# Kernel tuning notes

Hardware: AMD Instinct MI355X
Metric: run time of the kernel (lower is better)

## Reference

```python
import jax, jax.numpy as jnp
import numpy as np

N_BITS = 6
N_ENTRIES = 1 << N_BITS  # 64 LUT entries per node
B, IN, OUT = 1024, 1024, 2048


def setup_inputs() -> dict:
    key = jax.random.key(0)
    k1, k2, k3 = jax.random.split(key, 3)
    x = jax.random.uniform(k1, (B, IN), dtype=jnp.float32)          # soft bits in [0,1]
    lut_table = jax.random.normal(k2, (OUT, N_ENTRIES), dtype=jnp.float32)  # per-node LUT weights
    mapping = jax.random.randint(k3, (OUT, N_BITS), 0, IN, dtype=jnp.int32)  # wires per node
    return {"x": x, "lut_table": lut_table, "mapping": mapping}


def _lut_forward(x, lut_table, mapping):
    # get_mapping: gather n input wires per output node -> [B, OUT, n]
    mapped = x[:, mapping]
    # bits[k, j] = j-th bit of entry k  -> [2^n, n]
    bits = ((jnp.arange(N_ENTRIES)[:, None] >> jnp.arange(N_BITS)[None, :]) & 1
            ).astype(x.dtype)
    # Soft-AND probability of each LUT entry, built multiplicatively over the
    # n (=6) fan-in bits to avoid a [B,OUT,2^n,n] intermediate.
    probs = jnp.ones((x.shape[0], mapping.shape[0], N_ENTRIES), dtype=x.dtype)
    for j in range(N_BITS):
        xj = mapped[:, :, j][:, :, None]              # [B, OUT, 1]
        bj = bits[:, j][None, None, :]                # [1, 1, 2^n]
        probs = probs * (bj * xj + (1.0 - bj) * (1.0 - xj))
    # Expected LUT output per node: contract entry axis with learned table.
    return jnp.einsum('bok,ok->bo', probs, lut_table)


def reference(x, lut_table, mapping):
    return _lut_forward(x, lut_table, mapping)
```

## Files before the change

kernel.cpp:

```cpp
#include <hip/hip_runtime.h>

#define B_DIM   1024
#define IN_DIM  1024
#define OUT_DIM 2048
#define NBITS   6
#define NENT    64

#define OB   256
#define BB   16
#define LROW 65

__global__ __launch_bounds__(256, 2) void lut_fused(
    const float* __restrict__ x,
    const float* __restrict__ lut,
    const int*   __restrict__ mapping,
    float*       __restrict__ out)
{
    __shared__ __align__(16) float smem[OB * LROW];
    const int tid = threadIdx.x;
    const int o0  = blockIdx.x * OB;
    const int b0  = blockIdx.y * BB;
    const int o   = o0 + tid;

    const float4* lsrc = (const float4*)(lut + (size_t)o0 * NENT);
#pragma unroll
    for (int i = 0; i < (OB * NENT / 4) / 256; i++) {
        const int f   = i * 256 + tid;
        const float4 val = lsrc[f];
        const int ow  = f >> 4;
        const int kw  = (f & 15) * 4;
        float* d = &smem[ow * LROW + kw];
        d[0] = val.x; d[1] = val.y; d[2] = val.z; d[3] = val.w;
    }

    int mp[NBITS];
#pragma unroll
    for (int j = 0; j < NBITS; j++) mp[j] = mapping[(size_t)o * NBITS + j];

    __syncthreads();

    float v[NENT];
#pragma unroll
    for (int k = 0; k < NENT; k++) v[k] = smem[tid * LROW + k];

#pragma unroll
    for (int j = 0; j < NBITS; j++) {
#pragma unroll
        for (int k = 0; k < NENT; k++) {
            if ((k >> j) & 1) v[k] -= v[k ^ (1 << j)];
        }
    }

    __syncthreads();

    const float4* xsrc = (const float4*)(x + (size_t)b0 * IN_DIM);
    float4* xdst = (float4*)smem;
#pragma unroll
    for (int i = 0; i < (BB * IN_DIM / 4) / 256; i++) {
        const int f = i * 256 + tid;
        xdst[f] = xsrc[f];
    }
    __syncthreads();

#pragma unroll 4
    for (int bi = 0; bi < BB; bi++) {
        const float* xr = &smem[bi * IN_DIM];
        float xv[NBITS];
#pragma unroll
        for (int j = 0; j < NBITS; j++) xv[j] = xr[mp[j]];

        float w[NENT / 2];
        {
            const float xj = xv[0];
#pragma unroll
            for (int m = 0; m < NENT / 2; m++)
                w[m] = fmaf(xj, v[2 * m + 1], v[2 * m]);
        }
#pragma unroll
        for (int j = 1; j < NBITS; j++) {
            const float xj = xv[j];
#pragma unroll
            for (int m = 0; m < (NENT >> (j + 1)); m++)
                w[m] = fmaf(xj, w[2 * m + 1], w[2 * m]);
        }
        out[(size_t)(b0 + bi) * OUT_DIM + o] = w[0];
    }
}

extern "C" void kernel_launch(void* const* d_in, const int* in_sizes, int n_in,
                              void* d_out, int out_size, void* d_ws, size_t ws_size,
                              hipStream_t stream) {
    const float* x       = (const float*)d_in[0];
    const float* lut     = (const float*)d_in[1];
    const int*   mapping = (const int*)d_in[2];
    float*       out     = (float*)d_out;
    (void)d_ws; (void)ws_size;

    const dim3 grid(OUT_DIM / OB, B_DIM / BB);
    lut_fused<<<grid, 256, 0, stream>>>(x, lut, mapping, out);
}
```

Measured before the change: 69.45 us.

## Load LUT rows directly into registers and overlap x staging with transform

Each thread now reads its own 64-entry LUT row straight from global memory as float4 into registers, so the padded shared-memory staging of the table and one barrier are gone. The x tile copy into shared memory is issued first so it overlaps with the LUT load and the per-thread Möbius transform, leaving one sync. Shared memory per block shrinks, and the batch loop unroll drops from 4 to 2. The per-thread row reads are strided across lanes (256 B apart), which may coalesce worse than the old cooperative copy.

Measured after the change: 70.93 us. 2.1% more time.

```diff
diff --git a/kernel.cpp b/kernel.cpp
--- a/kernel.cpp
+++ b/kernel.cpp
@@ -8,7 +8,6 @@
 
 #define OB   256
 #define BB   16
-#define LROW 65
 
 __global__ __launch_bounds__(256, 2) void lut_fused(
     const float* __restrict__ x,
@@ -16,32 +15,34 @@
     const int*   __restrict__ mapping,
     float*       __restrict__ out)
 {
-    __shared__ __align__(16) float smem[OB * LROW];
+    __shared__ __align__(16) float sx[BB * IN_DIM];
     const int tid = threadIdx.x;
     const int o0  = blockIdx.x * OB;
     const int b0  = blockIdx.y * BB;
     const int o   = o0 + tid;
 
-    const float4* lsrc = (const float4*)(lut + (size_t)o0 * NENT);
+    const float4* xsrc = (const float4*)(x + (size_t)b0 * IN_DIM);
+    float4* xdst = (float4*)sx;
 #pragma unroll
-    for (int i = 0; i < (OB * NENT / 4) / 256; i++) {
-        const int f   = i * 256 + tid;
-        const float4 val = lsrc[f];
-        const int ow  = f >> 4;
-        const int kw  = (f & 15) * 4;
-        float* d = &smem[ow * LROW + kw];
-        d[0] = val.x; d[1] = val.y; d[2] = val.z; d[3] = val.w;
+    for (int i = 0; i < (BB * IN_DIM / 4) / OB; i++) {
+        const int f = i * OB + tid;
+        xdst[f] = xsrc[f];
+    }
+
+    float v[NENT];
+    {
+        const float4* lr = (const float4*)(lut + (size_t)o * NENT);
+#pragma unroll
+        for (int q = 0; q < NENT / 4; q++) {
+            const float4 t = lr[q];
+            v[4 * q + 0] = t.x; v[4 * q + 1] = t.y;
+            v[4 * q + 2] = t.z; v[4 * q + 3] = t.w;
+        }
     }
 
     int mp[NBITS];
 #pragma unroll
     for (int j = 0; j < NBITS; j++) mp[j] = mapping[(size_t)o * NBITS + j];
-
-    __syncthreads();
-
-    float v[NENT];
-#pragma unroll
-    for (int k = 0; k < NENT; k++) v[k] = smem[tid * LROW + k];
 
 #pragma unroll
     for (int j = 0; j < NBITS; j++) {
@@ -53,18 +54,9 @@
 
     __syncthreads();
 
-    const float4* xsrc = (const float4*)(x + (size_t)b0 * IN_DIM);
-    float4* xdst = (float4*)smem;
-#pragma unroll
-    for (int i = 0; i < (BB * IN_DIM / 4) / 256; i++) {
-        const int f = i * 256 + tid;
-        xdst[f] = xsrc[f];
-    }
-    __syncthreads();
-
-#pragma unroll 4
+#pragma unroll 2
     for (int bi = 0; bi < BB; bi++) {
-        const float* xr = &smem[bi * IN_DIM];
+        const float* xr = &sx[bi * IN_DIM];
         float xv[NBITS];
 #pragma unroll
         for (int j = 0; j < NBITS; j++) xv[j] = xr[mp[j]];
```
